# Kernel optimization log

Hardware: AMD Instinct MI355X
Metric: run time of the kernel (lower is better)

Reference implementation:

```python
import jax, jax.numpy as jnp
import numpy as np

APP = 21  # app_num, hard-coded in the original forward (x[..., -21:])


def setup_inputs() -> dict:
    key = jax.random.key(0)
    S, F = 1024, 64            # seq_len, feature_num
    INP = F - 21 + 1           # input_size = 44
    H, E = 1024, 512           # hidden_size, embedding_size
    OUT = 1
    ks = jax.random.split(key, 16)
    s = 0.02
    return {
        "x": jax.random.normal(ks[0], (1, S, F), jnp.float32),
        "W_ie": jax.random.normal(ks[1], (E, INP), jnp.float32) * s,
        "b_ie": jnp.zeros((E,), jnp.float32),
        "W_te": jax.random.normal(ks[2], (E, APP * H), jnp.float32) * s,
        "b_te": jnp.zeros((E,), jnp.float32),
        "W_ih0": jax.random.normal(ks[3], (4 * H, 2 * E), jnp.float32) * s,
        "W_hh0": jax.random.normal(ks[4], (4 * H, H), jnp.float32) * s,
        "b_ih0": jnp.zeros((4 * H,), jnp.float32),
        "b_hh0": jnp.zeros((4 * H,), jnp.float32),
        "W_ih1": jax.random.normal(ks[5], (4 * H, H), jnp.float32) * s,
        "W_hh1": jax.random.normal(ks[6], (4 * H, H), jnp.float32) * s,
        "b_ih1": jnp.zeros((4 * H,), jnp.float32),
        "b_hh1": jnp.zeros((4 * H,), jnp.float32),
        "W_out": jax.random.normal(ks[7], (OUT, APP * H), jnp.float32) * s,
        "b_out": jnp.zeros((OUT,), jnp.float32),
    }


def _lstm_cell(xt, h, c, W_ih, W_hh, b_ih, b_hh):
    # PyTorch gate order: i, f, g, o
    gates = xt @ W_ih.T + b_ih + h @ W_hh.T + b_hh  # [APP, 4H]
    i, f, g, o = jnp.split(gates, 4, axis=-1)
    c_new = jax.nn.sigmoid(f) * c + jax.nn.sigmoid(i) * jnp.tanh(g)
    h_new = jax.nn.sigmoid(o) * jnp.tanh(c_new)
    return h_new, c_new


def reference(x, W_ie, b_ie, W_te, b_te, W_ih0, W_hh0, b_ih0, b_hh0,
              W_ih1, W_hh1, b_ih1, b_hh1, W_out, b_out):
    # eval-mode: dropout is identity (both embedding dropout and LSTM inter-layer dropout)
    S = x.shape[1]
    H = W_hh0.shape[1]
    E = W_ie.shape[0]

    feats = x[0, :, :-APP]                                   # [S, F-21]
    feats = jnp.broadcast_to(feats[:, None, :], (S, APP, feats.shape[-1]))
    app = x[0, :, -APP:][:, :, None]                          # [S, 21, 1]
    input_data = jnp.concatenate([feats, app], axis=-1)       # [S, 21, INP]

    h0 = jnp.zeros((APP, H), x.dtype)
    c0 = jnp.zeros((APP, H), x.dtype)
    h1 = jnp.zeros((APP, H), x.dtype)
    c1 = jnp.zeros((APP, H), x.dtype)

    def step(carry, xt):
        h0, c0, h1, c1 = carry
        # social tensor: last-layer hidden flattened, identical row for all 21 apps
        social = h1.reshape(-1)                               # [21*H]
        te = jax.nn.relu(W_te @ social + b_te)                # [E]
        ie = jax.nn.relu(xt @ W_ie.T + b_ie)                  # [21, E]
        z = jnp.concatenate([ie, jnp.broadcast_to(te, (APP, E))], axis=-1)  # [21, 2E]
        h0n, c0n = _lstm_cell(z, h0, c0, W_ih0, W_hh0, b_ih0, b_hh0)
        h1n, c1n = _lstm_cell(h0n, h1, c1, W_ih1, W_hh1, b_ih1, b_hh1)
        out = W_out @ h1n.reshape(-1) + b_out                 # [output_size]
        return (h0n, c0n, h1n, c1n), out

    (h0, c0, h1, c1), outs = jax.lax.scan(step, (h0, c0, h1, c1), input_data)
    outputs = outs[None, :, :]                                # [1, S, output_size]
    hidden = jnp.stack([h0, h1], axis=0)                      # [num_layer, 21, H]
    cell = jnp.stack([c0, c1], axis=0)
    return outputs, (hidden, cell)
```

## Files before the change

### kernel.cpp

```cpp
#include <hip/hip_runtime.h>
#include <math.h>


#define NBLK 256
#define NTHR 512
#define HTHR 256
#define SEQ  1024
#define HID  1024
#define EMB  512
#define NAG  21
#define NH   21504

#define IE_OFF  0
#define H0_OFF  11010048
#define TE_OFF  (H0_OFF + 43008)
#define BAR_OFF (TE_OFF + 512)
#define ZTOT    (43008 + 512 + 1024)

#define HROW   1152
#define IEROW  576
#define OFF_H    0
#define OFF_IE   24192
#define OFF_TE   36288
#define OFF_PART 36864
#define OFF_B0   39888
#define OFF_B1   39904
#define OFF_RED  39920
#define OFF_ABT  39936
#define LDS_F    39952

#define REP4(M)  M(0) M(1) M(2) M(3)
#define REP5(M)  REP4(M) M(4)
#define REP8(M)  REP4(M) M(4) M(5) M(6) M(7)
#define REP16(M) REP8(M) M(8) M(9) M(10) M(11) M(12) M(13) M(14) M(15)
#define REP20(M) REP16(M) M(16) M(17) M(18) M(19)
#define REP40(M) REP20(M) M(20) M(21) M(22) M(23) \
  M(24) M(25) M(26) M(27) M(28) M(29) M(30) M(31) M(32) M(33) M(34) M(35) \
  M(36) M(37) M(38) M(39)

typedef unsigned u32x4 __attribute__((ext_vector_type(4)));

struct Params {
  const float *x, *W_ie, *b_ie, *W_te, *b_te;
  const float *W_ih0, *W_hh0, *b_ih0, *b_hh0;
  const float *W_ih1, *W_hh1, *b_ih1, *b_hh1;
  const float *W_out, *b_out;
  float *out, *ws;
};

__device__ __forceinline__ float sigf(float v) { return 1.0f / (1.0f + expf(-v)); }
__device__ __forceinline__ float bfl(unsigned u) { return __uint_as_float(u << 16); }
__device__ __forceinline__ float bfh(unsigned u) { return __uint_as_float(u & 0xffff0000u); }
__device__ __forceinline__ unsigned f2bf(float f) {
  unsigned u = __float_as_uint(f);
  return (u + 0x7fffu + ((u >> 16) & 1u)) >> 16;
}

__device__ __forceinline__ float block_sum(float v, float* red) {
  #pragma unroll
  for (int off = 32; off > 0; off >>= 1) v += __shfl_down(v, off, 64);
  const int w = threadIdx.x >> 6;
  if ((threadIdx.x & 63) == 0) red[w] = v;
  __syncthreads();
  float r = 0.f;
  #pragma unroll
  for (int i = 0; i < NTHR / 64; ++i) r += red[i];
  __syncthreads();
  return r;
}

__device__ __forceinline__ void block_sum2(float& v0, float& v1, float* red) {
  #pragma unroll
  for (int off = 32; off > 0; off >>= 1) {
    v0 += __shfl_down(v0, off, 64);
    v1 += __shfl_down(v1, off, 64);
  }
  const int w = threadIdx.x >> 6;
  if ((threadIdx.x & 63) == 0) { red[2 * w] = v0; red[2 * w + 1] = v1; }
  __syncthreads();
  v0 = ((red[0] + red[2]) + (red[4] + red[6])) + ((red[8] + red[10]) + (red[12] + red[14]));
  v1 = ((red[1] + red[3]) + (red[5] + red[7])) + ((red[9] + red[11]) + (red[13] + red[15]));
  __syncthreads();
}

__device__ __forceinline__ bool grid_barrier(unsigned* bars, unsigned ep, int b,
                                             float* ldsf) {
  __syncthreads();
  if (threadIdx.x == 0) {
    float abortv = 0.f;
    unsigned* grel = bars + 512 + ((unsigned)b >> 4) * 32;
    if (__hip_atomic_load(bars + 300, __ATOMIC_RELAXED, __HIP_MEMORY_SCOPE_AGENT) != 0u) {
      abortv = 1.f;
    } else {
      asm volatile("s_waitcnt vmcnt(0)" ::: "memory");
      unsigned* gc = bars + 16 + ((unsigned)b >> 4) * 16;
      unsigned old = __hip_atomic_fetch_add(gc, 1u, __ATOMIC_RELAXED, __HIP_MEMORY_SCOPE_AGENT);
      if (old == ep * 16u - 1u) {
        unsigned rold = __hip_atomic_fetch_add(bars + 16 + 256, 1u, __ATOMIC_RELAXED, __HIP_MEMORY_SCOPE_AGENT);
        if (rold == ep * 16u - 1u) {
          #pragma unroll
          for (int g = 0; g < 16; ++g)
            __hip_atomic_store(bars + 512 + g * 32, ep, __ATOMIC_RELAXED, __HIP_MEMORY_SCOPE_AGENT);
        }
      }
      unsigned spins = 0u;
      while (__hip_atomic_load(grel, __ATOMIC_RELAXED, __HIP_MEMORY_SCOPE_AGENT) < ep) {
        __builtin_amdgcn_s_sleep(8);
        if (++spins > 1000000u) {
          __hip_atomic_store(bars + 300, 1u, __ATOMIC_RELAXED, __HIP_MEMORY_SCOPE_AGENT);
          abortv = 1.f;
          break;
        }
        if ((spins & 255u) == 0u &&
            __hip_atomic_load(bars + 300, __ATOMIC_RELAXED, __HIP_MEMORY_SCOPE_AGENT) != 0u) {
          abortv = 1.f;
          break;
        }
      }
      asm volatile("" ::: "memory");
    }
    ldsf[OFF_ABT] = abortv;
  }
  __syncthreads();
  return ldsf[OFF_ABT] != 0.f;
}

__global__ void sl_init(float* ws) {
  int tid = blockIdx.x * blockDim.x + threadIdx.x;
  int stride = gridDim.x * blockDim.x;
  for (int i = tid; i < ZTOT; i += stride) ws[H0_OFF + i] = 0.0f;
}

__global__ void sl_ie(const float* __restrict__ x, const float* __restrict__ W_ie,
                      const float* __restrict__ b_ie, float* __restrict__ ws) {
  const int t = blockIdx.x;
  const int tid = threadIdx.x;
  __shared__ float xs[64];
  __shared__ float base[EMB];
  __shared__ float w43[EMB];
  if (tid < 64) xs[tid] = x[t * 64 + tid];
  __syncthreads();
  for (int e = tid; e < EMB; e += HTHR) {
    const float* wr = W_ie + e * 44;
    float acc = b_ie[e];
    #pragma unroll
    for (int k = 0; k < 43; ++k) acc += xs[k] * wr[k];
    base[e] = acc;
    w43[e] = wr[43];
  }
  __syncthreads();
  float* iep = ws + IE_OFF + (size_t)t * (NAG * EMB);
  for (int idx = tid; idx < NAG * EMB; idx += HTHR) {
    int a = idx >> 9, e = idx & 511;
    float v = base[e] + xs[43 + a] * w43[e];
    iep[idx] = v > 0.0f ? v : 0.0f;
  }
}

#define HBLD(q) { const u32x4* ap = (const u32x4*)(srcu + 20 * tid) + (q); \
  asm volatile("global_load_dwordx4 %0, %1, off sc0" : "=v"(sv[q]) : "v"(ap)); }
#define ST2(u, e0) { int aa = (e0) >> 10; int cc = (e0) & 1023; float2 f2v; \
  f2v.x = bfl(u); f2v.y = bfh(u); \
  *(float2*)&lds[OFF_H + aa * HROW + 36 * (cc >> 5) + (cc & 31)] = f2v; }
#define HBST(q) { ST2(sv[q][0], 40*tid + 8*(q)) ST2(sv[q][1], 40*tid + 8*(q)+2) \
  ST2(sv[q][2], 40*tid + 8*(q)+4) ST2(sv[q][3], 40*tid + 8*(q)+6) }
#define STAGE_HBF(SRCU) { \
  const unsigned* srcu = (SRCU); \
  u32x4 sv[5]; unsigned sv2; \
  REP5(HBLD) \
  { const unsigned* ap = srcu + 10240 + tid; \
    asm volatile("global_load_dword %0, %1, off sc0" : "=v"(sv2) : "v"(ap)); } \
  asm volatile("s_waitcnt vmcnt(0)" ::: "memory"); \
  __builtin_amdgcn_sched_barrier(0); \
  REP5(HBST) \
  ST2(sv2, 20480 + 2 * tid) }

__global__ void __launch_bounds__(NTHR)
__attribute__((amdgpu_waves_per_eu(2, 2)))
sl_main(Params P) {
  const int b = blockIdx.x;
  const int tid = threadIdx.x;
  float* ws = P.ws;
  float* wste = ws + TE_OFF;
  unsigned* hbase = (unsigned*)(ws + H0_OFF);
  unsigned* bars = (unsigned*)(ws + BAR_OFF);

  __shared__ float lds[LDS_F];

  const int lane = tid & 63;
  const int wav  = tid >> 6;
  const int n    = tid & 15;
  const int ks   = tid >> 4;
  const int grow = (n >> 2) * HID + 4 * b + (n & 3);

  float w0[64];
  {
    const float* s0 = (ks < 16) ? (P.W_ih0 + (size_t)grow * 1024 + 64 * ks)
                                : (P.W_hh0 + (size_t)grow * 1024 + 64 * (ks - 16));
#define LW0(i) { float4 v = *(const float4*)(s0 + 4*(i)); \
    w0[4*(i)] = v.x; w0[4*(i)+1] = v.y; w0[4*(i)+2] = v.z; w0[4*(i)+3] = v.w; }
    REP16(LW0)
  }
  float w1a[32], w1b[32];
  {
    const float* s1 = P.W_ih1 + (size_t)grow * 1024 + 32 * ks;
    const float* s2 = P.W_hh1 + (size_t)grow * 1024 + 32 * ks;
#define LW1(i) { float4 v = *(const float4*)(s1 + 4*(i)); \
    w1a[4*(i)] = v.x; w1a[4*(i)+1] = v.y; w1a[4*(i)+2] = v.z; w1a[4*(i)+3] = v.w; \
    float4 u = *(const float4*)(s2 + 4*(i)); \
    w1b[4*(i)] = u.x; w1b[4*(i)+1] = u.y; w1b[4*(i)+2] = u.z; w1b[4*(i)+3] = u.w; }
    REP8(LW1)
  }
  unsigned wtepk[42];
  {
    const float* wt0 = P.W_te + (size_t)(2 * b) * NH;
#define LWT(k) { float f0 = wt0[40*tid + (k)]; float f1 = wt0[NH + 40*tid + (k)]; \
    wtepk[k] = f2bf(f0) | (f2bf(f1) << 16); }
    REP40(LWT)
    { int ix = 20480 + 2 * tid;
      wtepk[40] = f2bf(wt0[ix])     | (f2bf(wt0[NH + ix]) << 16);
      wtepk[41] = f2bf(wt0[ix + 1]) | (f2bf(wt0[NH + ix + 1]) << 16); }
  }
  const float bte0 = P.b_te[2 * b], bte1 = P.b_te[2 * b + 1];
  const float bout = P.b_out[0];
  if (tid < 16) {
    int gr = (tid >> 2) * HID + 4 * b + (tid & 3);
    lds[OFF_B0 + tid] = P.b_ih0[gr] + P.b_hh0[gr];
    lds[OFF_B1 + tid] = P.b_ih1[gr] + P.b_hh1[gr];
  }
  __syncthreads();

  int bB_base, bB_astep;
  if (ks < 8)       { bB_base = OFF_IE + 72 * ks;        bB_astep = IEROW; }
  else if (ks < 16) { bB_base = OFF_TE + 72 * (ks - 8);  bB_astep = 0;     }
  else              { bB_base = OFF_H  + 72 * (ks - 16); bB_astep = HROW;  }
  const int bC_base = OFF_H + 36 * ks;

  float c0r = 0.f, c1r = 0.f, h0r = 0.f, h1r = 0.f;
  unsigned ep = 0;

  for (int t = 0; t < SEQ; ++t) {
    const int p = t & 1;
    u32x4 hv[5]; unsigned hv2;

    {
      const unsigned* h1u = hbase + 21504 + p * 10752;
#define PALD(q) { const u32x4* ap = (const u32x4*)(h1u + 20 * tid) + (q); \
      asm volatile("global_load_dwordx4 %0, %1, off sc0" : "=v"(hv[q]) : "v"(ap)); }
      REP5(PALD)
      { const unsigned* ap = h1u + 10240 + tid;
        asm volatile("global_load_dword %0, %1, off sc0" : "=v"(hv2) : "v"(ap)); }
      asm volatile("s_waitcnt vmcnt(0)" ::: "memory");
      __builtin_amdgcn_sched_barrier(0);
      float a0 = 0.f, a1 = 0.f;
#define PHAF(k) { unsigned hu = hv[(k) >> 3][((k) >> 1) & 3]; \
      float hvf = ((k) & 1) ? bfh(hu) : bfl(hu); \
      a0 += bfl(wtepk[k]) * hvf; \
      a1 += bfh(wtepk[k]) * hvf; }
      REP40(PHAF)
      { float hvf = bfl(hv2);
        a0 += bfl(wtepk[40]) * hvf; a1 += bfh(wtepk[40]) * hvf; }
      { float hvf = bfh(hv2);
        a0 += bfl(wtepk[41]) * hvf; a1 += bfh(wtepk[41]) * hvf; }
      block_sum2(a0, a1, &lds[OFF_RED]);
      if (tid == 0) {
        float v0 = a0 + bte0, v1 = a1 + bte1;
        v0 = v0 > 0.f ? v0 : 0.f;
        v1 = v1 > 0.f ? v1 : 0.f;
        unsigned long long tv = ((unsigned long long)__float_as_uint(v1) << 32)
                              | (unsigned long long)__float_as_uint(v0);
        __hip_atomic_store((unsigned long long*)(wste + 2 * b), tv,
                           __ATOMIC_RELAXED, __HIP_MEMORY_SCOPE_AGENT);
      }
      if (b == 0) {
        float ao = 0.f;
        if (t > 0) {
#define PAO(m) { float2 wv = *(const float2*)(P.W_out + 40 * tid + 2 * (m)); \
          unsigned hu = hv[(m) >> 2][(m) & 3]; \
          ao += wv.x * bfl(hu) + wv.y * bfh(hu); }
          REP20(PAO)
          const float* woe = P.W_out + 20480 + 2 * tid;
          ao += woe[0] * bfl(hv2) + woe[1] * bfh(hv2);
        }
        ao = block_sum(ao, &lds[OFF_RED]);
        if (tid == 0 && t > 0) P.out[t - 1] = ao + bout;
      }
    }
    ++ep; if (grid_barrier(bars, ep, b, lds)) break;

    {
      float tev;
      { const float* ap = wste + tid;
        asm volatile("global_load_dword %0, %1, off sc0" : "=v"(tev) : "v"(ap)); }
      {
        const float4* iep4 =
            (const float4*)(ws + IE_OFF + (size_t)t * (NAG * EMB));
        float4 t40 = iep4[tid];
        float4 t41 = iep4[tid + 512];
        float4 t42 = iep4[tid + 1024];
        float4 t43 = iep4[tid + 1536];
        float4 t44 = iep4[tid + 2048];
        float4 t45 = t40;
        const bool g5 = tid < 128;
        if (g5) t45 = iep4[tid + 2560];
#define IEST(k, reg) { int i4 = tid + 512*(k); int aa = i4 >> 7; int k4 = i4 & 127; \
        *(float4*)&lds[OFF_IE + aa * IEROW + 36 * (k4 >> 3) + 4 * (k4 & 7)] = reg; }
        IEST(0, t40) IEST(1, t41) IEST(2, t42) IEST(3, t43) IEST(4, t44)
        if (g5) IEST(5, t45)
      }
      STAGE_HBF(hbase + p * 10752)
      lds[OFF_TE + 36 * (tid >> 5) + (tid & 31)] = tev;
      __syncthreads();

      int laddr = bB_base;
      for (int a = 0; a < NAG; ++a) {
        float ac0 = 0.f, ac1 = 0.f, ac2 = 0.f, ac3 = 0.f;
#define DOTB(j, ac, woff, zoff) { float4 z = *(const float4*)&lds[laddr + (zoff) + 4*(j)]; \
        ac += w0[(woff)+4*(j)]*z.x;   ac += w0[(woff)+4*(j)+1]*z.y; \
        ac += w0[(woff)+4*(j)+2]*z.z; ac += w0[(woff)+4*(j)+3]*z.w; }
        DOTB(0, ac0, 0, 0)  DOTB(1, ac1, 0, 0)  DOTB(2, ac2, 0, 0)  DOTB(3, ac3, 0, 0)
        DOTB(4, ac0, 0, 0)  DOTB(5, ac1, 0, 0)  DOTB(6, ac2, 0, 0)  DOTB(7, ac3, 0, 0)
        DOTB(0, ac0, 32, 36) DOTB(1, ac1, 32, 36) DOTB(2, ac2, 32, 36) DOTB(3, ac3, 32, 36)
        DOTB(4, ac0, 32, 36) DOTB(5, ac1, 32, 36) DOTB(6, ac2, 32, 36) DOTB(7, ac3, 32, 36)
        float acc = (ac0 + ac1) + (ac2 + ac3);
        acc += __shfl_xor(acc, 16);
        acc += __shfl_xor(acc, 32);
        if (lane < 16) lds[OFF_PART + a * 144 + n * 9 + wav] = acc;
        laddr += bB_astep;
      }
      __syncthreads();
      if (tid < 84) {
        int a = tid >> 2, j = tid & 3;
        const float* pp = &lds[OFF_PART + a * 144];
        float gv0, gv1, gv2, gv3;
#define GATE(base, gg, gv) { float s = lds[(base) + 4*(gg) + j]; \
        s += pp[(4*(gg)+j)*9+0] + pp[(4*(gg)+j)*9+1] + pp[(4*(gg)+j)*9+2] + pp[(4*(gg)+j)*9+3]; \
        s += pp[(4*(gg)+j)*9+4] + pp[(4*(gg)+j)*9+5] + pp[(4*(gg)+j)*9+6] + pp[(4*(gg)+j)*9+7]; \
        gv = s; }
        GATE(OFF_B0, 0, gv0) GATE(OFF_B0, 1, gv1) GATE(OFF_B0, 2, gv2) GATE(OFF_B0, 3, gv3)
        float cn = sigf(gv1) * c0r + sigf(gv0) * tanhf(gv2);
        float hn = sigf(gv3) * tanhf(cn);
        c0r = cn; h0r = hn;
        unsigned hb16 = f2bf(hn);
        unsigned nb1 = __shfl_down(hb16, 1, 64);
        unsigned nb2 = __shfl_down(hb16, 2, 64);
        unsigned nb3 = __shfl_down(hb16, 3, 64);
        if (j == 0) {
          unsigned long long pk = (unsigned long long)hb16
            | ((unsigned long long)nb1 << 16) | ((unsigned long long)nb2 << 32)
            | ((unsigned long long)nb3 << 48);
          __hip_atomic_store((unsigned long long*)(hbase + (p ^ 1) * 10752) + (a * 256 + b),
                             pk, __ATOMIC_RELAXED, __HIP_MEMORY_SCOPE_AGENT);
        }
      }
    }
    ++ep; if (grid_barrier(bars, ep, b, lds)) break;

    {
      STAGE_HBF(hbase + (p ^ 1) * 10752)
      __syncthreads();
      int laddr = bC_base;
      for (int a = 0; a < NAG; ++a) {
        float ac0 = 0.f, ac1 = 0.f;
#define DOTC(j, ac, W) { float4 z = *(const float4*)&lds[laddr + 4*(j)]; \
        ac += W[4*(j)]*z.x; ac += W[4*(j)+1]*z.y; ac += W[4*(j)+2]*z.z; ac += W[4*(j)+3]*z.w; }
        DOTC(0, ac0, w1a) DOTC(1, ac1, w1a) DOTC(2, ac0, w1a) DOTC(3, ac1, w1a)
        DOTC(4, ac0, w1a) DOTC(5, ac1, w1a) DOTC(6, ac0, w1a) DOTC(7, ac1, w1a)
        float acc = ac0 + ac1;
        acc += __shfl_xor(acc, 16);
        acc += __shfl_xor(acc, 32);
        if (lane < 16) lds[OFF_PART + a * 144 + n * 9 + wav] = acc;
        laddr += HROW;
      }
      __syncthreads();
      {
#define RSTB(q) { ST2(hv[q][0], 40*tid + 8*(q)) ST2(hv[q][1], 40*tid + 8*(q)+2) \
        ST2(hv[q][2], 40*tid + 8*(q)+4) ST2(hv[q][3], 40*tid + 8*(q)+6) }
        REP5(RSTB)
        ST2(hv2, 20480 + 2 * tid)
      }
      __syncthreads();
      laddr = bC_base;
      for (int a = 0; a < NAG; ++a) {
        float ac0 = 0.f, ac1 = 0.f;
        DOTC(0, ac0, w1b) DOTC(1, ac1, w1b) DOTC(2, ac0, w1b) DOTC(3, ac1, w1b)
        DOTC(4, ac0, w1b) DOTC(5, ac1, w1b) DOTC(6, ac0, w1b) DOTC(7, ac1, w1b)
        float acc = ac0 + ac1;
        acc += __shfl_xor(acc, 16);
        acc += __shfl_xor(acc, 32);
        if (lane < 16) lds[OFF_PART + a * 144 + n * 9 + wav] += acc;
        laddr += HROW;
      }
      __syncthreads();
      if (tid < 84) {
        int a = tid >> 2, j = tid & 3;
        const float* pp = &lds[OFF_PART + a * 144];
        float gv0, gv1, gv2, gv3;
        GATE(OFF_B1, 0, gv0) GATE(OFF_B1, 1, gv1) GATE(OFF_B1, 2, gv2) GATE(OFF_B1, 3, gv3)
        float cn = sigf(gv1) * c1r + sigf(gv0) * tanhf(gv2);
        float hn = sigf(gv3) * tanhf(cn);
        c1r = cn; h1r = hn;
        unsigned hb16 = f2bf(hn);
        unsigned nb1 = __shfl_down(hb16, 1, 64);
        unsigned nb2 = __shfl_down(hb16, 2, 64);
        unsigned nb3 = __shfl_down(hb16, 3, 64);
        if (j == 0) {
          unsigned long long pk = (unsigned long long)hb16
            | ((unsigned long long)nb1 << 16) | ((unsigned long long)nb2 << 32)
            | ((unsigned long long)nb3 << 48);
          __hip_atomic_store((unsigned long long*)(hbase + 21504 + (p ^ 1) * 10752) + (a * 256 + b),
                             pk, __ATOMIC_RELAXED, __HIP_MEMORY_SCOPE_AGENT);
        }
      }
    }
    ++ep; if (grid_barrier(bars, ep, b, lds)) break;
  }

  if (b == 0) {
    const unsigned* h1u = hbase + 21504;
    u32x4 ev[5]; unsigned ev2;
#define ELD(q) { const u32x4* ap = (const u32x4*)(h1u + 20 * tid) + (q); \
    asm volatile("global_load_dwordx4 %0, %1, off sc0" : "=v"(ev[q]) : "v"(ap)); }
    REP5(ELD)
    { const unsigned* ap = h1u + 10240 + tid;
      asm volatile("global_load_dword %0, %1, off sc0" : "=v"(ev2) : "v"(ap)); }
    asm volatile("s_waitcnt vmcnt(0)" ::: "memory");
    __builtin_amdgcn_sched_barrier(0);
    float ao = 0.f;
#define EAO(m) { float2 wv = *(const float2*)(P.W_out + 40 * tid + 2 * (m)); \
    unsigned hu = ev[(m) >> 2][(m) & 3]; \
    ao += wv.x * bfl(hu) + wv.y * bfh(hu); }
    REP20(EAO)
    { const float* woe = P.W_out + 20480 + 2 * tid;
      ao += woe[0] * bfl(ev2) + woe[1] * bfh(ev2); }
    ao = block_sum(ao, &lds[OFF_RED]);
    if (tid == 0) P.out[SEQ - 1] = ao + bout;
  }
  if (tid < 84) {
    int a = tid >> 2, j = tid & 3;
    int idx = a * HID + 4 * b + j;
    P.out[SEQ + idx]          = h0r;
    P.out[SEQ + NH + idx]     = h1r;
    P.out[SEQ + 2*NH + idx]   = c0r;
    P.out[SEQ + 3*NH + idx]   = c1r;
  }
}

extern "C" void kernel_launch(void* const* d_in, const int* in_sizes, int n_in,
                              void* d_out, int out_size, void* d_ws, size_t ws_size,
                              hipStream_t stream) {
  (void)in_sizes; (void)n_in; (void)out_size; (void)ws_size;
  Params P;
  P.x     = (const float*)d_in[0];
  P.W_ie  = (const float*)d_in[1];
  P.b_ie  = (const float*)d_in[2];
  P.W_te  = (const float*)d_in[3];
  P.b_te  = (const float*)d_in[4];
  P.W_ih0 = (const float*)d_in[5];
  P.W_hh0 = (const float*)d_in[6];
  P.b_ih0 = (const float*)d_in[7];
  P.b_hh0 = (const float*)d_in[8];
  P.W_ih1 = (const float*)d_in[9];
  P.W_hh1 = (const float*)d_in[10];
  P.b_ih1 = (const float*)d_in[11];
  P.b_hh1 = (const float*)d_in[12];
  P.W_out = (const float*)d_in[13];
  P.b_out = (const float*)d_in[14];
  P.out   = (float*)d_out;
  P.ws    = (float*)d_ws;

  sl_init<<<64, HTHR, 0, stream>>>((float*)d_ws);
  sl_ie<<<SEQ, HTHR, 0, stream>>>(P.x, P.W_ie, P.b_ie, (float*)d_ws);

  void* args[] = { &P };
  hipLaunchCooperativeKernel((const void*)sl_main, dim3(NBLK), dim3(NTHR),
                             args, 0, stream);
}
```

Measured before the change: 52.51 ms.

## Store input embeddings as bf16 and reuse staged layer-0 hidden state across phases

The precomputed input-embedding buffer is now stored as packed bf16 pairs instead of fp32, which halves the global traffic when it is staged into LDS at each timestep. The h0 vector that phase C loads from global memory is kept in registers (cv) and reused in the next step's phase B, which removes one global reload of the hidden state per step. The cost is lower precision in the ie activations and extra register pressure from carrying the hidden-state vector across the grid barrier.

```diff
diff --git a/kernel.cpp b/kernel.cpp
--- a/kernel.cpp
+++ b/kernel.cpp
@@ -149,31 +149,20 @@
     w43[e] = wr[43];
   }
   __syncthreads();
-  float* iep = ws + IE_OFF + (size_t)t * (NAG * EMB);
-  for (int idx = tid; idx < NAG * EMB; idx += HTHR) {
-    int a = idx >> 9, e = idx & 511;
-    float v = base[e] + xs[43 + a] * w43[e];
-    iep[idx] = v > 0.0f ? v : 0.0f;
-  }
-}
-
-#define HBLD(q) { const u32x4* ap = (const u32x4*)(srcu + 20 * tid) + (q); \
-  asm volatile("global_load_dwordx4 %0, %1, off sc0" : "=v"(sv[q]) : "v"(ap)); }
+  unsigned* iep = (unsigned*)(ws + IE_OFF) + (size_t)t * 5376;
+  for (int i = tid; i < 5376; i += HTHR) {
+    int a = i >> 8, c2 = i & 255;
+    int e0 = 2 * c2, e1 = e0 + 1;
+    float xa = xs[43 + a];
+    float v0 = base[e0] + xa * w43[e0]; v0 = v0 > 0.f ? v0 : 0.f;
+    float v1 = base[e1] + xa * w43[e1]; v1 = v1 > 0.f ? v1 : 0.f;
+    iep[i] = f2bf(v0) | (f2bf(v1) << 16);
+  }
+}
+
 #define ST2(u, e0) { int aa = (e0) >> 10; int cc = (e0) & 1023; float2 f2v; \
   f2v.x = bfl(u); f2v.y = bfh(u); \
   *(float2*)&lds[OFF_H + aa * HROW + 36 * (cc >> 5) + (cc & 31)] = f2v; }
-#define HBST(q) { ST2(sv[q][0], 40*tid + 8*(q)) ST2(sv[q][1], 40*tid + 8*(q)+2) \
-  ST2(sv[q][2], 40*tid + 8*(q)+4) ST2(sv[q][3], 40*tid + 8*(q)+6) }
-#define STAGE_HBF(SRCU) { \
-  const unsigned* srcu = (SRCU); \
-  u32x4 sv[5]; unsigned sv2; \
-  REP5(HBLD) \
-  { const unsigned* ap = srcu + 10240 + tid; \
-    asm volatile("global_load_dword %0, %1, off sc0" : "=v"(sv2) : "v"(ap)); } \
-  asm volatile("s_waitcnt vmcnt(0)" ::: "memory"); \
-  __builtin_amdgcn_sched_barrier(0); \
-  REP5(HBST) \
-  ST2(sv2, 20480 + 2 * tid) }
 
 __global__ void __launch_bounds__(NTHR)
 __attribute__((amdgpu_waves_per_eu(2, 2)))
@@ -237,6 +226,8 @@
   const int bC_base = OFF_H + 36 * ks;
 
   float c0r = 0.f, c1r = 0.f, h0r = 0.f, h1r = 0.f;
+  u32x4 cv[5]; unsigned cv2 = 0u;
+  cv[0] = cv[1] = cv[2] = cv[3] = cv[4] = (u32x4){0u, 0u, 0u, 0u};
   unsigned ep = 0;
 
   for (int t = 0; t < SEQ; ++t) {
@@ -293,22 +284,26 @@
       { const float* ap = wste + tid;
         asm volatile("global_load_dword %0, %1, off sc0" : "=v"(tev) : "v"(ap)); }
       {
-        const float4* iep4 =
-            (const float4*)(ws + IE_OFF + (size_t)t * (NAG * EMB));
-        float4 t40 = iep4[tid];
-        float4 t41 = iep4[tid + 512];
-        float4 t42 = iep4[tid + 1024];
-        float4 t43 = iep4[tid + 1536];
-        float4 t44 = iep4[tid + 2048];
-        float4 t45 = t40;
-        const bool g5 = tid < 128;
-        if (g5) t45 = iep4[tid + 2560];
-#define IEST(k, reg) { int i4 = tid + 512*(k); int aa = i4 >> 7; int k4 = i4 & 127; \
-        *(float4*)&lds[OFF_IE + aa * IEROW + 36 * (k4 >> 3) + 4 * (k4 & 7)] = reg; }
-        IEST(0, t40) IEST(1, t41) IEST(2, t42) IEST(3, t43) IEST(4, t44)
-        if (g5) IEST(5, t45)
-      }
-      STAGE_HBF(hbase + p * 10752)
+        const u32x4* iequ = (const u32x4*)((const unsigned*)(ws + IE_OFF)
+                                           + (size_t)t * 5376);
+        u32x4 iv0 = iequ[tid];
+        u32x4 iv1 = iequ[tid + 512];
+        u32x4 iv2 = iv0;
+        const bool g2 = tid < 320;
+        if (g2) iv2 = iequ[tid + 1024];
+#define IEU(v, j) { int aa = (j) >> 6; int ch = ((j) >> 2) & 15; int of = 8 * ((j) & 3); \
+        float4 fA; fA.x = bfl(v[0]); fA.y = bfh(v[0]); fA.z = bfl(v[1]); fA.w = bfh(v[1]); \
+        float4 fB; fB.x = bfl(v[2]); fB.y = bfh(v[2]); fB.z = bfl(v[3]); fB.w = bfh(v[3]); \
+        float* pq = &lds[OFF_IE + aa * IEROW + 36 * ch + of]; \
+        *(float4*)pq = fA; *(float4*)(pq + 4) = fB; }
+        IEU(iv0, tid) IEU(iv1, tid + 512) if (g2) IEU(iv2, tid + 1024)
+      }
+      {
+#define CST(q) { ST2(cv[q][0], 40*tid + 8*(q)) ST2(cv[q][1], 40*tid + 8*(q)+2) \
+        ST2(cv[q][2], 40*tid + 8*(q)+4) ST2(cv[q][3], 40*tid + 8*(q)+6) }
+        REP5(CST)
+        ST2(cv2, 20480 + 2 * tid)
+      }
       lds[OFF_TE + 36 * (tid >> 5) + (tid & 31)] = tev;
       __syncthreads();
 
@@ -357,7 +352,18 @@
     ++ep; if (grid_barrier(bars, ep, b, lds)) break;
 
     {
-      STAGE_HBF(hbase + (p ^ 1) * 10752)
+      {
+        const unsigned* srcu = hbase + (p ^ 1) * 10752;
+#define CLD(q) { const u32x4* ap = (const u32x4*)(srcu + 20 * tid) + (q); \
+        asm volatile("global_load_dwordx4 %0, %1, off sc0" : "=v"(cv[q]) : "v"(ap)); }
+        REP5(CLD)
+        { const unsigned* ap = srcu + 10240 + tid;
+          asm volatile("global_load_dword %0, %1, off sc0" : "=v"(cv2) : "v"(ap)); }
+        asm volatile("s_waitcnt vmcnt(0)" ::: "memory");
+        __builtin_amdgcn_sched_barrier(0);
+        REP5(CST)
+        ST2(cv2, 20480 + 2 * tid)
+      }
       __syncthreads();
       int laddr = bC_base;
       for (int a = 0; a < NAG; ++a) {
```

New measurement: 54.91 ms. 4.6% more time.
